# Optimization experiments

Hardware: AMD Instinct MI355X
Metric: run time of the kernel (lower is better)

Reference implementation:

```python
import jax, jax.numpy as jnp
import numpy as np

B, N, D = 2, 4096, 2048
H, DH, W = 8, 128, 512          # heads (num_queries), dim_head, window_size
SCALE = 8.0                      # qk_scale (qk_rmsnorm=True)


def setup_inputs() -> dict:
    key = jax.random.key(0)
    ks = jax.random.split(key, 5)
    return {
        "x": jax.random.normal(ks[0], (B, N, D), jnp.float32),
        "Wq": jax.random.normal(ks[1], (H * DH, D), jnp.float32) * 0.02,
        "Wkv": jax.random.normal(ks[2], (2 * H * DH, D), jnp.float32) * 0.02,
        "q_scale": jnp.ones((DH,), jnp.float32),
        "k_scale": jnp.ones((DH,), jnp.float32),
        "Wg": jax.random.normal(ks[3], (H, D), jnp.float32) * 0.02,
        "bg": jnp.zeros((H,), jnp.float32),
        "Wo": jax.random.normal(ks[4], (D, H * DH), jnp.float32) * 0.02,
    }


def _l2norm(t):
    # F.normalize: x / max(||x||, eps)
    return t / jnp.maximum(jnp.linalg.norm(t, axis=-1, keepdims=True), 1e-12)


def reference(x, Wq, Wkv, q_scale, k_scale, Wg, bg, Wo):
    b, n, _ = x.shape
    inner = H * DH
    q = (x @ Wq.T).reshape(b, n, H, DH).transpose(0, 2, 1, 3)      # b h n d
    kv = x @ Wkv.T
    k = kv[..., :inner].reshape(b, n, H, DH).transpose(0, 2, 1, 3)
    v = kv[..., inner:].reshape(b, n, H, DH).transpose(0, 2, 1, 3)
    # qk rmsnorm
    q = _l2norm(q) * q_scale
    k = _l2norm(k) * k_scale

    nb = n // W
    qb = q.reshape(b, H, nb, W, DH)
    kb = k.reshape(b, H, nb, W, DH)
    vb = v.reshape(b, H, nb, W, DH)

    def look_around(t):  # prepend previous bucket (look_backward=1)
        prev = jnp.concatenate([jnp.zeros_like(t[:, :, :1]), t[:, :, :-1]], axis=2)
        return jnp.concatenate([prev, t], axis=3)  # b h nb 2W d

    kw, vw = look_around(kb), look_around(vb)

    pos = jnp.arange(n).reshape(nb, W)
    pos_prev = jnp.concatenate([jnp.full((1, W), -1), pos[:-1]], axis=0)
    posk = jnp.concatenate([pos_prev, pos], axis=1)                 # nb 2W
    dist = pos[:, :, None] - posk[:, None, :]                       # nb W 2W
    # causal + exact window: attend j with 0 <= i - j <= W, valid (non-pad) key
    mask = (posk[:, None, :] >= 0) & (dist >= 0) & (dist <= W)

    sim = jnp.einsum('bhnid,bhnjd->bhnij', qb * SCALE, kw)
    sim = jnp.where(mask, sim, jnp.finfo(sim.dtype).min)
    attn = jax.nn.softmax(sim, axis=-1)
    o = jnp.einsum('bhnij,bhnjd->bhnid', attn, vw).reshape(b, H, n, DH)

    # per-head sigmoid value gating
    gates = jax.nn.sigmoid(jnp.einsum('bnd,hd->bhn', x, Wg) + bg[None, :, None])
    o = o * gates[..., None]

    o = o.transpose(0, 2, 1, 3).reshape(b, n, inner)                # b n (h d)
    return o @ Wo.T
```

## Files before the change

kernel.cpp:

```cpp
#include <hip/hip_runtime.h>
#include <hip/hip_bf16.h>
#include <cstdint>

typedef short short8 __attribute__((ext_vector_type(8)));
typedef short short4v __attribute__((ext_vector_type(4)));
typedef __bf16 bf16x8 __attribute__((ext_vector_type(8)));
typedef float f32x4 __attribute__((ext_vector_type(4)));
typedef unsigned short u16;
typedef unsigned int u32;

#define B_  2
#define N_  4096
#define D_  2048
#define H_  8
#define DH_ 128
#define W_  512
#define M_  (B_*N_)
#define INNER_ (H_*DH_)

static __device__ __forceinline__ u16 f2bf(float f) {
  u32 u = __float_as_uint(f);
  u32 r = (u + 0x7fffu + ((u >> 16) & 1u)) >> 16;
  return (u16)r;
}
static __device__ __forceinline__ float bf2f(u16 u) {
  return __uint_as_float(((u32)u) << 16);
}
static __device__ __forceinline__ f32x4 mfma16(short8 a, short8 b, f32x4 c) {
  return __builtin_amdgcn_mfma_f32_16x16x32_bf16(
      __builtin_bit_cast(bf16x8, a), __builtin_bit_cast(bf16x8, b), c, 0, 0, 0);
}

#define GLOAD_LDS16(g, s) \
  __builtin_amdgcn_global_load_lds((const __attribute__((address_space(1))) void*)(g), \
                                   (__attribute__((address_space(3))) void*)(s), 16, 0, 0)

__global__ __launch_bounds__(256) void cvt_kernel(
    const float* __restrict__ x, const float* __restrict__ Wq,
    const float* __restrict__ Wkv, const float* __restrict__ Wo,
    u16* __restrict__ xb, u16* __restrict__ Wcat, u16* __restrict__ Wob) {
  size_t i = ((size_t)blockIdx.x * 256 + threadIdx.x) * 8;
  const float* src; u16* dst; size_t off;
  const size_t SX = 16777216ul, SQ = 2097152ul, SKV = 4194304ul;
  if (i < SX)                { src = x;   dst = xb;             off = i; }
  else if (i < SX+SQ)        { src = Wq;  dst = Wcat;           off = i - SX; }
  else if (i < SX+SQ+SKV)    { src = Wkv; dst = Wcat + 2097152; off = i - SX - SQ; }
  else                       { src = Wo;  dst = Wob;            off = i - SX - SQ - SKV; }
  float4 a = *(const float4*)(src + off);
  float4 b = *(const float4*)(src + off + 4);
  short8 o;
  o[0]=(short)f2bf(a.x); o[1]=(short)f2bf(a.y); o[2]=(short)f2bf(a.z); o[3]=(short)f2bf(a.w);
  o[4]=(short)f2bf(b.x); o[5]=(short)f2bf(b.y); o[6]=(short)f2bf(b.z); o[7]=(short)f2bf(b.w);
  *(short8*)(dst + off) = o;
}

template<int EPI>
__global__ __launch_bounds__(256) void gemm_bt(
    const u16* __restrict__ A, const u16* __restrict__ Bw,
    u16* __restrict__ Dst, float* __restrict__ Cf,
    const float* __restrict__ sc, int K) {
  __shared__ u16 sA[128*64];
  __shared__ u16 sB[128*64];
  __shared__ float pbuf[2][128];
  const int tid = threadIdx.x;
  const int lane = tid & 63, wv = tid >> 6;
  const int wm = wv >> 1, wn = wv & 1;
  const int m0 = blockIdx.y * 128, n0 = blockIdx.x * 128;
  const int l15 = lane & 15, l4 = lane >> 4;
  f32x4 acc[4][4] = {};

  #pragma unroll 1
  for (int kt = 0; kt < K; kt += 64) {
    __syncthreads();
    #pragma unroll
    for (int r = 0; r < 4; ++r) {
      int cf = r*256 + tid;
      int row = cf >> 3, cph = cf & 7;
      int clg = cph ^ (row & 7);
      GLOAD_LDS16(A + (size_t)(m0 + row)*K + kt + clg*8, sA + (size_t)(r*256 + wv*64)*8);
    }
    #pragma unroll
    for (int r = 0; r < 4; ++r) {
      int cf = r*256 + tid;
      int row = cf >> 3, cph = cf & 7;
      int clg = cph ^ (row & 7);
      GLOAD_LDS16(Bw + (size_t)(n0 + row)*K + kt + clg*8, sB + (size_t)(r*256 + wv*64)*8);
    }
    __syncthreads();
    #pragma unroll
    for (int ks = 0; ks < 2; ++ks) {
      short8 af[4], bfr[4];
      #pragma unroll
      for (int mf = 0; mf < 4; ++mf) {
        int row = wm*64 + mf*16 + l15;
        int ch = (ks*4 + l4) ^ (row & 7);
        af[mf] = *(const short8*)(sA + row*64 + ch*8);
      }
      #pragma unroll
      for (int nf = 0; nf < 4; ++nf) {
        int row = wn*64 + nf*16 + l15;
        int ch = (ks*4 + l4) ^ (row & 7);
        bfr[nf] = *(const short8*)(sB + row*64 + ch*8);
      }
      #pragma unroll
      for (int mf = 0; mf < 4; ++mf)
        #pragma unroll
        for (int nf = 0; nf < 4; ++nf)
          acc[mf][nf] = mfma16(af[mf], bfr[nf], acc[mf][nf]);
    }
  }

  if (EPI <= 1) {
    #pragma unroll
    for (int mf = 0; mf < 4; ++mf)
      #pragma unroll
      for (int j = 0; j < 4; ++j) {
        float ss = acc[mf][0][j]*acc[mf][0][j] + acc[mf][1][j]*acc[mf][1][j]
                 + acc[mf][2][j]*acc[mf][2][j] + acc[mf][3][j]*acc[mf][3][j];
        #pragma unroll
        for (int off = 1; off <= 8; off <<= 1) ss += __shfl_xor(ss, off);
        if (l15 == 0) pbuf[wn][wm*64 + mf*16 + l4*4 + j] = ss;
      }
    __syncthreads();
    const int h = blockIdx.x;
    const int b = m0 >> 12;
    #pragma unroll
    for (int mf = 0; mf < 4; ++mf)
      #pragma unroll
      for (int j = 0; j < 4; ++j) {
        int rloc = wm*64 + mf*16 + l4*4 + j;
        float ss = pbuf[0][rloc] + pbuf[1][rloc];
        float inv = 1.0f / fmaxf(sqrtf(ss), 1e-12f);
        if (EPI == 0) inv *= 8.0f;
        int n = (m0 + rloc) & (N_ - 1);
        size_t base = ((size_t)(b*H_ + h)*N_ + n) << 7;
        #pragma unroll
        for (int nf = 0; nf < 4; ++nf) {
          int d = wn*64 + nf*16 + l15;
          Dst[base + d] = f2bf(acc[mf][nf][j] * inv * sc[d]);
        }
      }
  } else if (EPI == 2) {
    const int h = blockIdx.x;
    const int b = m0 >> 12;
    const int bh = b*H_ + h;
    #pragma unroll
    for (int mf = 0; mf < 4; ++mf)
      #pragma unroll
      for (int nf = 0; nf < 4; ++nf) {
        int d = wn*64 + nf*16 + l15;
        int n = ((m0 & (N_ - 1)) + wm*64 + mf*16 + l4*4);
        short4v pk;
        pk[0] = (short)f2bf(acc[mf][nf][0]);
        pk[1] = (short)f2bf(acc[mf][nf][1]);
        pk[2] = (short)f2bf(acc[mf][nf][2]);
        pk[3] = (short)f2bf(acc[mf][nf][3]);
        *(short4v*)(Dst + ((size_t)bh*128 + d)*N_ + n) = pk;
      }
  } else {
    #pragma unroll
    for (int mf = 0; mf < 4; ++mf)
      #pragma unroll
      for (int nf = 0; nf < 4; ++nf)
        #pragma unroll
        for (int j = 0; j < 4; ++j) {
          int m = m0 + wm*64 + mf*16 + l4*4 + j;
          int nn = n0 + wn*64 + nf*16 + l15;
          Cf[(size_t)m*D_ + nn] = acc[mf][nf][j];
        }
  }
}

__global__ __launch_bounds__(256) void gates_kernel(
    const u16* __restrict__ xb, const float* __restrict__ Wg,
    const float* __restrict__ bg, float* __restrict__ gates) {
  int m = blockIdx.x;
  int tid = threadIdx.x;
  const u16* xr = xb + (size_t)m * D_;
  float acc[8] = {};
  for (int d0 = tid*8; d0 < D_; d0 += 256*8) {
    short8 xv8 = *(const short8*)(xr + d0);
    #pragma unroll
    for (int e = 0; e < 8; ++e) {
      float xv = bf2f((u16)xv8[e]);
      #pragma unroll
      for (int h = 0; h < 8; ++h) acc[h] = fmaf(xv, Wg[h*D_ + d0 + e], acc[h]);
    }
  }
  #pragma unroll
  for (int h = 0; h < 8; ++h)
    #pragma unroll
    for (int off = 32; off >= 1; off >>= 1) acc[h] += __shfl_xor(acc[h], off);
  __shared__ float red[4][8];
  int lane = tid & 63, wv = tid >> 6;
  if (lane == 0) {
    #pragma unroll
    for (int h = 0; h < 8; ++h) red[wv][h] = acc[h];
  }
  __syncthreads();
  if (tid < 8) {
    float vsum = red[0][tid] + red[1][tid] + red[2][tid] + red[3][tid] + bg[tid];
    gates[(size_t)m*8 + tid] = 1.0f / (1.0f + __expf(-vsum));
  }
}

__global__ __launch_bounds__(256) void attn_kernel(
    const u16* __restrict__ q, const u16* __restrict__ k,
    const u16* __restrict__ vT, const float* __restrict__ gates,
    u16* __restrict__ o) {
  const int bid = blockIdx.x;
  const int t = bid & 3;
  const int c = (bid >> 2) & 7;
  const int bh = bid >> 5;
  const int b = bh >> 3, h = bh & 7;
  const int i0 = c*W_ + t*128;
  const int tid = threadIdx.x;
  const int lane = tid & 63, wv = tid >> 6;
  const int l15 = lane & 15, l4 = lane >> 4;

  __shared__ u16 sK[64*128];
  __shared__ u16 sV[128*64];
  __shared__ u16 sP[4][32*64];

  short8 qf[2][4];
  const u16* qbase = q + (((size_t)bh*N_ + i0 + wv*32) << 7);
  #pragma unroll
  for (int mf = 0; mf < 2; ++mf)
    #pragma unroll
    for (int ks = 0; ks < 4; ++ks)
      qf[mf][ks] = *(const short8*)(qbase + (mf*16 + l15)*128 + ks*32 + l4*8);

  float mrow[2][4], lrow[2][4];
  f32x4 oacc[2][8];
  #pragma unroll
  for (int mf = 0; mf < 2; ++mf) {
    #pragma unroll
    for (int j = 0; j < 4; ++j) { mrow[mf][j] = -1e30f; lrow[mf][j] = 0.f; }
    #pragma unroll
    for (int df = 0; df < 8; ++df) oacc[mf][df] = (f32x4){0.f,0.f,0.f,0.f};
  }
  u16* sPw = &sP[wv][0];

  #pragma unroll 1
  for (int kt = 0; kt < 10; ++kt) {
    const int j0 = i0 - 512 + kt*64;
    if (j0 < 0) continue;
    __syncthreads();
    #pragma unroll
    for (int r = 0; r < 4; ++r) {
      int cf = r*256 + tid;
      int row = cf >> 4, cph = cf & 15;
      int clg = cph ^ (row & 15);
      GLOAD_LDS16(k + (((size_t)bh*N_ + j0 + row) << 7) + clg*8, sK + (size_t)(r*256 + wv*64)*8);
    }
    #pragma unroll
    for (int r = 0; r < 4; ++r) {
      int cf = r*256 + tid;
      int row = cf >> 3, cph = cf & 7;
      int clg = cph ^ (row & 7);
      GLOAD_LDS16(vT + ((size_t)bh*128 + row)*N_ + j0 + clg*8, sV + (size_t)(r*256 + wv*64)*8);
    }
    __syncthreads();

    const int base = 512 - kt*64;
    const int rmin = wv*32;
    if (base + rmin + 31 < 0 || base + rmin - 63 > 512) continue;

    f32x4 s[2][4];
    #pragma unroll
    for (int mf = 0; mf < 2; ++mf)
      #pragma unroll
      for (int nf = 0; nf < 4; ++nf) s[mf][nf] = (f32x4){0.f,0.f,0.f,0.f};
    #pragma unroll
    for (int ks = 0; ks < 4; ++ks) {
      short8 kb[4];
      #pragma unroll
      for (int nf = 0; nf < 4; ++nf) {
        int row = nf*16 + l15;
        int ch = (ks*4 + l4) ^ (row & 15);
        kb[nf] = *(const short8*)(sK + row*128 + ch*8);
      }
      #pragma unroll
      for (int mf = 0; mf < 2; ++mf)
        #pragma unroll
        for (int nf = 0; nf < 4; ++nf)
          s[mf][nf] = mfma16(qf[mf][ks], kb[nf], s[mf][nf]);
    }

    if (kt < 2 || kt > 7) {
      #pragma unroll
      for (int mf = 0; mf < 2; ++mf)
        #pragma unroll
        for (int nf = 0; nf < 4; ++nf)
          #pragma unroll
          for (int j = 0; j < 4; ++j) {
            int r = wv*32 + mf*16 + l4*4 + j;
            int sidx = nf*16 + l15;
            int dist = (i0 + r) - (j0 + sidx);
            if (dist < 0 || dist > 512) s[mf][nf][j] = -1e30f;
          }
    }

    #pragma unroll
    for (int mf = 0; mf < 2; ++mf) {
      #pragma unroll
      for (int j = 0; j < 4; ++j) {
        float mx = fmaxf(fmaxf(s[mf][0][j], s[mf][1][j]), fmaxf(s[mf][2][j], s[mf][3][j]));
        #pragma unroll
        for (int off = 1; off <= 8; off <<= 1) mx = fmaxf(mx, __shfl_xor(mx, off));
        float mnew = fmaxf(mrow[mf][j], mx);
        float scal = __expf(mrow[mf][j] - mnew);
        mrow[mf][j] = mnew;
        float ls = 0.f;
        #pragma unroll
        for (int nf = 0; nf < 4; ++nf) {
          float p = __expf(s[mf][nf][j] - mnew);
          s[mf][nf][j] = p;
          ls += p;
        }
        #pragma unroll
        for (int off = 1; off <= 8; off <<= 1) ls += __shfl_xor(ls, off);
        lrow[mf][j] = lrow[mf][j]*scal + ls;
        #pragma unroll
        for (int df = 0; df < 8; ++df) oacc[mf][df][j] *= scal;
        int prow = mf*16 + l4*4 + j;
        #pragma unroll
        for (int nf = 0; nf < 4; ++nf) {
          int pcol = nf*16 + l15;
          int ch = (pcol >> 3) ^ (prow & 7);
          sPw[prow*64 + ch*8 + (pcol & 7)] = f2bf(s[mf][nf][j]);
        }
      }
    }

    #pragma unroll
    for (int ks2 = 0; ks2 < 2; ++ks2) {
      short8 pa[2];
      #pragma unroll
      for (int mf = 0; mf < 2; ++mf) {
        int prow = mf*16 + l15;
        int ch = (ks2*4 + l4) ^ (prow & 7);
        pa[mf] = *(const short8*)(sPw + prow*64 + ch*8);
      }
      #pragma unroll
      for (int df = 0; df < 8; ++df) {
        int vd = df*16 + l15;
        int ch2 = (ks2*4 + l4) ^ (vd & 7);
        short8 vb = *(const short8*)(sV + vd*64 + ch2*8);
        #pragma unroll
        for (int mf = 0; mf < 2; ++mf)
          oacc[mf][df] = mfma16(pa[mf], vb, oacc[mf][df]);
      }
    }
  }

  #pragma unroll
  for (int mf = 0; mf < 2; ++mf)
    #pragma unroll
    for (int j = 0; j < 4; ++j) {
      int r = wv*32 + mf*16 + l4*4 + j;
      int i = i0 + r;
      float f = (1.0f / lrow[mf][j]) * gates[((size_t)b*N_ + i)*8 + h];
      #pragma unroll
      for (int df = 0; df < 8; ++df)
        o[((size_t)b*N_ + i)*INNER_ + h*128 + df*16 + l15] = f2bf(oacc[mf][df][j] * f);
    }
}

extern "C" void kernel_launch(void* const* d_in, const int* in_sizes, int n_in,
                              void* d_out, int out_size, void* d_ws, size_t ws_size,
                              hipStream_t stream) {
  const float* x       = (const float*)d_in[0];
  const float* Wq      = (const float*)d_in[1];
  const float* Wkv     = (const float*)d_in[2];
  const float* q_scale = (const float*)d_in[3];
  const float* k_scale = (const float*)d_in[4];
  const float* Wg      = (const float*)d_in[5];
  const float* bg      = (const float*)d_in[6];
  const float* Wo      = (const float*)d_in[7];
  float* out = (float*)d_out;

  u16* qb  = (u16*)d_out;
  u16* kb  = qb + 8388608;
  u16* vTb = kb + 8388608;

  char* w = (char*)d_ws;
  u16* xb   = (u16*)w;
  u16* ob   = (u16*)w;
  u16* Wcat = (u16*)(w + 33554432);
  u16* Wob  = (u16*)(w + 46137344);
  float* gb = (float*)(w + 50331648);
  (void)in_sizes; (void)n_in; (void)out_size; (void)ws_size;

  cvt_kernel<<<12288, 256, 0, stream>>>(x, Wq, Wkv, Wo, xb, Wcat, Wob);
  gemm_bt<0><<<dim3(8, 64), 256, 0, stream>>>(xb, Wcat,                       qb,  nullptr, q_scale, 2048);
  gemm_bt<1><<<dim3(8, 64), 256, 0, stream>>>(xb, Wcat + (size_t)1024*2048,   kb,  nullptr, k_scale, 2048);
  gemm_bt<2><<<dim3(8, 64), 256, 0, stream>>>(xb, Wcat + (size_t)2048*2048,   vTb, nullptr, nullptr, 2048);
  gates_kernel<<<8192, 256, 0, stream>>>(xb, Wg, bg, gb);
  attn_kernel<<<512, 256, 0, stream>>>(qb, kb, vTb, gb, ob);
  gemm_bt<3><<<dim3(16, 64), 256, 0, stream>>>(ob, Wob, nullptr, out, nullptr, 1024);
}
```

Measured before the change: 323.5 us.

## Double-buffer K/V tiles in attention with 8 waves and lazy softmax rescale

The attention kernel now runs 512 threads (8 waves of 16 query rows each) instead of 4 waves of 32 rows. K/V tiles are double-buffered in dynamic LDS, with the next tile prefetched while the current one is computed, and synchronisation uses explicit vmcnt waits and raw barriers. The online softmax skips the rescale of the running max unless a row max grows by more than 8. This aims to hide global load latency and cut rescale work, at the cost of more LDS (80KB) and fragile manual waitcnt logic.

```diff
diff --git a/kernel.cpp b/kernel.cpp
--- a/kernel.cpp
+++ b/kernel.cpp
@@ -34,6 +34,10 @@
 #define GLOAD_LDS16(g, s) \
   __builtin_amdgcn_global_load_lds((const __attribute__((address_space(1))) void*)(g), \
                                    (__attribute__((address_space(3))) void*)(s), 16, 0, 0)
+#define BARRIER() __builtin_amdgcn_s_barrier()
+#define SB0 __builtin_amdgcn_sched_barrier(0)
+#define WVM4 asm volatile("s_waitcnt vmcnt(4)" ::: "memory")
+#define WVM0 asm volatile("s_waitcnt vmcnt(0)" ::: "memory")
 
 __global__ __launch_bounds__(256) void cvt_kernel(
     const float* __restrict__ x, const float* __restrict__ Wq,
@@ -204,10 +208,13 @@
   }
 }
 
-__global__ __launch_bounds__(256) void attn_kernel(
+__global__ __launch_bounds__(512, 4) void attn_kernel(
     const u16* __restrict__ q, const u16* __restrict__ k,
     const u16* __restrict__ vT, const float* __restrict__ gates,
     u16* __restrict__ o) {
+  extern __shared__ u16 alds[];
+  u16* sK = alds;
+  u16* sV = alds + 16384;
   const int bid = blockIdx.x;
   const int t = bid & 3;
   const int c = (bid >> 2) & 7;
@@ -217,154 +224,143 @@
   const int tid = threadIdx.x;
   const int lane = tid & 63, wv = tid >> 6;
   const int l15 = lane & 15, l4 = lane >> 4;
-
-  __shared__ u16 sK[64*128];
-  __shared__ u16 sV[128*64];
-  __shared__ u16 sP[4][32*64];
-
-  short8 qf[2][4];
-  const u16* qbase = q + (((size_t)bh*N_ + i0 + wv*32) << 7);
+  u16* sPw = alds + 32768 + wv*1024;
+
+#define STAGE_KV(KT, PB) do { \
+    const int _j0 = i0 - 512 + (KT)*64; \
+    u16* _dK = sK + (PB)*8192; \
+    u16* _dV = sV + (PB)*8192; \
+    _Pragma("unroll") for (int r = 0; r < 2; ++r) { \
+      int cf = r*512 + tid; int row = cf >> 4, cph = cf & 15; \
+      int clg = cph ^ (row & 15); \
+      GLOAD_LDS16(k + (((size_t)bh*N_ + _j0 + row) << 7) + clg*8, _dK + (size_t)(r*512 + wv*64)*8); \
+    } \
+    _Pragma("unroll") for (int r = 0; r < 2; ++r) { \
+      int cf = r*512 + tid; int row = cf >> 3, cph = cf & 7; \
+      int clg = cph ^ (row & 7); \
+      GLOAD_LDS16(vT + ((size_t)bh*128 + row)*N_ + _j0 + clg*8, _dV + (size_t)(r*512 + wv*64)*8); \
+    } \
+  } while(0)
+
+  short8 qf[4];
+  const u16* qbase = q + (((size_t)bh*N_ + i0 + wv*16) << 7);
   #pragma unroll
-  for (int mf = 0; mf < 2; ++mf)
-    #pragma unroll
-    for (int ks = 0; ks < 4; ++ks)
-      qf[mf][ks] = *(const short8*)(qbase + (mf*16 + l15)*128 + ks*32 + l4*8);
-
-  float mrow[2][4], lrow[2][4];
-  f32x4 oacc[2][8];
+  for (int ks = 0; ks < 4; ++ks)
+    qf[ks] = *(const short8*)(qbase + l15*128 + ks*32 + l4*8);
+
+  float mrow[4], lrow[4];
+  f32x4 oacc[8];
   #pragma unroll
-  for (int mf = 0; mf < 2; ++mf) {
-    #pragma unroll
-    for (int j = 0; j < 4; ++j) { mrow[mf][j] = -1e30f; lrow[mf][j] = 0.f; }
-    #pragma unroll
-    for (int df = 0; df < 8; ++df) oacc[mf][df] = (f32x4){0.f,0.f,0.f,0.f};
-  }
-  u16* sPw = &sP[wv][0];
+  for (int j = 0; j < 4; ++j) { mrow[j] = -1e30f; lrow[j] = 0.f; }
+  #pragma unroll
+  for (int df = 0; df < 8; ++df) oacc[df] = (f32x4){0.f,0.f,0.f,0.f};
+
+  const int kt0 = (i0 >= 512) ? 0 : ((512 - i0) >> 6);
+  STAGE_KV(kt0, 0);
 
   #pragma unroll 1
-  for (int kt = 0; kt < 10; ++kt) {
-    const int j0 = i0 - 512 + kt*64;
-    if (j0 < 0) continue;
-    __syncthreads();
-    #pragma unroll
-    for (int r = 0; r < 4; ++r) {
-      int cf = r*256 + tid;
-      int row = cf >> 4, cph = cf & 15;
-      int clg = cph ^ (row & 15);
-      GLOAD_LDS16(k + (((size_t)bh*N_ + j0 + row) << 7) + clg*8, sK + (size_t)(r*256 + wv*64)*8);
-    }
-    #pragma unroll
-    for (int r = 0; r < 4; ++r) {
-      int cf = r*256 + tid;
-      int row = cf >> 3, cph = cf & 7;
-      int clg = cph ^ (row & 7);
-      GLOAD_LDS16(vT + ((size_t)bh*128 + row)*N_ + j0 + clg*8, sV + (size_t)(r*256 + wv*64)*8);
-    }
-    __syncthreads();
+  for (int kt = kt0; kt < 10; ++kt) {
+    const int pb = (kt - kt0) & 1;
+    if (kt < 9) { STAGE_KV(kt + 1, pb ^ 1); WVM4; } else { WVM0; }
+    BARRIER(); SB0;
 
     const int base = 512 - kt*64;
-    const int rmin = wv*32;
-    if (base + rmin + 31 < 0 || base + rmin - 63 > 512) continue;
-
-    f32x4 s[2][4];
-    #pragma unroll
-    for (int mf = 0; mf < 2; ++mf)
-      #pragma unroll
-      for (int nf = 0; nf < 4; ++nf) s[mf][nf] = (f32x4){0.f,0.f,0.f,0.f};
-    #pragma unroll
-    for (int ks = 0; ks < 4; ++ks) {
-      short8 kb[4];
-      #pragma unroll
-      for (int nf = 0; nf < 4; ++nf) {
-        int row = nf*16 + l15;
-        int ch = (ks*4 + l4) ^ (row & 15);
-        kb[nf] = *(const short8*)(sK + row*128 + ch*8);
-      }
-      #pragma unroll
-      for (int mf = 0; mf < 2; ++mf)
+    const int rmin = wv*16;
+    if (base + rmin + 15 >= 0 && base + rmin - 63 <= 512) {
+      const u16* cK = sK + pb*8192;
+      const u16* cV = sV + pb*8192;
+
+      f32x4 s[4];
+      #pragma unroll
+      for (int nf = 0; nf < 4; ++nf) s[nf] = (f32x4){0.f,0.f,0.f,0.f};
+      #pragma unroll
+      for (int ks = 0; ks < 4; ++ks) {
+        short8 kb[4];
+        #pragma unroll
+        for (int nf = 0; nf < 4; ++nf) {
+          int row = nf*16 + l15;
+          int ch = (ks*4 + l4) ^ (row & 15);
+          kb[nf] = *(const short8*)(cK + row*128 + ch*8);
+        }
         #pragma unroll
         for (int nf = 0; nf < 4; ++nf)
-          s[mf][nf] = mfma16(qf[mf][ks], kb[nf], s[mf][nf]);
-    }
-
-    if (kt < 2 || kt > 7) {
-      #pragma unroll
-      for (int mf = 0; mf < 2; ++mf)
+          s[nf] = mfma16(qf[ks], kb[nf], s[nf]);
+      }
+
+      if (kt < 2 || kt > 7) {
         #pragma unroll
         for (int nf = 0; nf < 4; ++nf)
           #pragma unroll
           for (int j = 0; j < 4; ++j) {
-            int r = wv*32 + mf*16 + l4*4 + j;
+            int r = rmin + l4*4 + j;
             int sidx = nf*16 + l15;
-            int dist = (i0 + r) - (j0 + sidx);
-            if (dist < 0 || dist > 512) s[mf][nf][j] = -1e30f;
+            int dist = base + r - sidx;
+            if (dist < 0 || dist > 512) s[nf][j] = -1e30f;
           }
-    }
-
-    #pragma unroll
-    for (int mf = 0; mf < 2; ++mf) {
+      }
+
       #pragma unroll
       for (int j = 0; j < 4; ++j) {
-        float mx = fmaxf(fmaxf(s[mf][0][j], s[mf][1][j]), fmaxf(s[mf][2][j], s[mf][3][j]));
+        float mx = fmaxf(fmaxf(s[0][j], s[1][j]), fmaxf(s[2][j], s[3][j]));
         #pragma unroll
         for (int off = 1; off <= 8; off <<= 1) mx = fmaxf(mx, __shfl_xor(mx, off));
-        float mnew = fmaxf(mrow[mf][j], mx);
-        float scal = __expf(mrow[mf][j] - mnew);
-        mrow[mf][j] = mnew;
+        if (!__all(mx <= mrow[j] + 8.0f)) {
+          float mnew = fmaxf(mrow[j], mx);
+          float scal = __expf(mrow[j] - mnew);
+          mrow[j] = mnew;
+          lrow[j] *= scal;
+          #pragma unroll
+          for (int df = 0; df < 8; ++df) oacc[df][j] *= scal;
+        }
+        float m = mrow[j];
         float ls = 0.f;
         #pragma unroll
         for (int nf = 0; nf < 4; ++nf) {
-          float p = __expf(s[mf][nf][j] - mnew);
-          s[mf][nf][j] = p;
+          float p = __expf(s[nf][j] - m);
+          s[nf][j] = p;
           ls += p;
         }
         #pragma unroll
         for (int off = 1; off <= 8; off <<= 1) ls += __shfl_xor(ls, off);
-        lrow[mf][j] = lrow[mf][j]*scal + ls;
-        #pragma unroll
-        for (int df = 0; df < 8; ++df) oacc[mf][df][j] *= scal;
-        int prow = mf*16 + l4*4 + j;
+        lrow[j] += ls;
+        int prow = l4*4 + j;
         #pragma unroll
         for (int nf = 0; nf < 4; ++nf) {
           int pcol = nf*16 + l15;
           int ch = (pcol >> 3) ^ (prow & 7);
-          sPw[prow*64 + ch*8 + (pcol & 7)] = f2bf(s[mf][nf][j]);
+          sPw[prow*64 + ch*8 + (pcol & 7)] = f2bf(s[nf][j]);
+        }
+      }
+
+      #pragma unroll
+      for (int ks2 = 0; ks2 < 2; ++ks2) {
+        short8 pa;
+        {
+          int ch = (ks2*4 + l4) ^ (l15 & 7);
+          pa = *(const short8*)(sPw + l15*64 + ch*8);
+        }
+        #pragma unroll
+        for (int df = 0; df < 8; ++df) {
+          int vd = df*16 + l15;
+          int ch2 = (ks2*4 + l4) ^ (vd & 7);
+          short8 vb = *(const short8*)(cV + vd*64 + ch2*8);
+          oacc[df] = mfma16(pa, vb, oacc[df]);
         }
       }
     }
-
-    #pragma unroll
-    for (int ks2 = 0; ks2 < 2; ++ks2) {
-      short8 pa[2];
-      #pragma unroll
-      for (int mf = 0; mf < 2; ++mf) {
-        int prow = mf*16 + l15;
-        int ch = (ks2*4 + l4) ^ (prow & 7);
-        pa[mf] = *(const short8*)(sPw + prow*64 + ch*8);
-      }
-      #pragma unroll
-      for (int df = 0; df < 8; ++df) {
-        int vd = df*16 + l15;
-        int ch2 = (ks2*4 + l4) ^ (vd & 7);
-        short8 vb = *(const short8*)(sV + vd*64 + ch2*8);
-        #pragma unroll
-        for (int mf = 0; mf < 2; ++mf)
-          oacc[mf][df] = mfma16(pa[mf], vb, oacc[mf][df]);
-      }
-    }
+    BARRIER();
   }
 
   #pragma unroll
-  for (int mf = 0; mf < 2; ++mf)
-    #pragma unroll
-    for (int j = 0; j < 4; ++j) {
-      int r = wv*32 + mf*16 + l4*4 + j;
-      int i = i0 + r;
-      float f = (1.0f / lrow[mf][j]) * gates[((size_t)b*N_ + i)*8 + h];
-      #pragma unroll
-      for (int df = 0; df < 8; ++df)
-        o[((size_t)b*N_ + i)*INNER_ + h*128 + df*16 + l15] = f2bf(oacc[mf][df][j] * f);
-    }
+  for (int j = 0; j < 4; ++j) {
+    int r = wv*16 + l4*4 + j;
+    int i = i0 + r;
+    float f = (1.0f / lrow[j]) * gates[((size_t)b*N_ + i)*8 + h];
+    #pragma unroll
+    for (int df = 0; df < 8; ++df)
+      o[((size_t)b*N_ + i)*INNER_ + h*128 + df*16 + l15] = f2bf(oacc[df][j] * f);
+  }
+#undef STAGE_KV
 }
 
 extern "C" void kernel_launch(void* const* d_in, const int* in_sizes, int n_in,
@@ -392,11 +388,14 @@
   float* gb = (float*)(w + 50331648);
   (void)in_sizes; (void)n_in; (void)out_size; (void)ws_size;
 
+  hipFuncSetAttribute((const void*)attn_kernel,
+                      hipFuncAttributeMaxDynamicSharedMemorySize, 81920);
+
   cvt_kernel<<<12288, 256, 0, stream>>>(x, Wq, Wkv, Wo, xb, Wcat, Wob);
   gemm_bt<0><<<dim3(8, 64), 256, 0, stream>>>(xb, Wcat,                       qb,  nullptr, q_scale, 2048);
   gemm_bt<1><<<dim3(8, 64), 256, 0, stream>>>(xb, Wcat + (size_t)1024*2048,   kb,  nullptr, k_scale, 2048);
   gemm_bt<2><<<dim3(8, 64), 256, 0, stream>>>(xb, Wcat + (size_t)2048*2048,   vTb, nullptr, nullptr, 2048);
   gates_kernel<<<8192, 256, 0, stream>>>(xb, Wg, bg, gb);
-  attn_kernel<<<512, 256, 0, stream>>>(qb, kb, vTb, gb, ob);
+  attn_kernel<<<512, 512, 81920, stream>>>(qb, kb, vTb, gb, ob);
   gemm_bt<3><<<dim3(16, 64), 256, 0, stream>>>(ob, Wob, nullptr, out, nullptr, 1024);
 }
```

Measured after the change: 288.7 us. -10.7%, faster.
